# Optimization experiments

Measured on AMD Instinct MI355X. Metric: run time of the kernel, lower is better.

The kernel has to match this reference:

```python
import math
import jax, jax.numpy as jnp
import numpy as np

B, T, L, H = 4, 4096, 4096, 1024


def setup_inputs() -> dict:
    key = jax.random.key(0)
    ks = jax.random.split(key, 12)
    inp = {
        "hidden_states": jax.random.normal(ks[0], (B, T, H), jnp.float32),
        "advisor_states": jax.random.normal(ks[1], (B, L, H), jnp.float32),
        "advisor_ids": jax.random.randint(ks[2], (B, L), 0, 8, jnp.int32),
        "pointer_ids": jax.random.randint(ks[3], (B, T), 0, L - 2, jnp.int32),
    }
    s = 1.0 / math.sqrt(H)
    names = ["Wqj", "Wkj", "Wvj", "Wqi", "Wki", "Wvi", "Wout"]
    for i, n in enumerate(names):
        inp[n] = jax.random.normal(ks[4 + i], (H, H), jnp.float32) * s
    inp["gain"] = jnp.asarray(0.1, jnp.float32)
    inp["council_weights"] = jnp.ones((2,), jnp.float32)
    return inp


def _forward(hidden_states, advisor_states, advisor_ids, pointer_ids,
             Wqj, Wkj, Wvj, Wqi, Wki, Wvi, Wout, gain, council_weights):
    b, t, h = hidden_states.shape
    l = advisor_states.shape[1]
    inv_sqrt_h = 1.0 / math.sqrt(float(h))

    # 3-token advisor window gather: indices [b, t, 3]
    p = pointer_ids[:, :, None]
    indices = jnp.clip(jnp.concatenate([p, p + 1, p + 2], axis=-1), 0, l - 1)
    win_states = jax.vmap(lambda a, idx: a[idx])(advisor_states, indices)  # [b,t,3,h]
    win_ids = jax.vmap(lambda a, idx: a[idx])(advisor_ids, indices)        # [b,t,3]

    # judge head
    qj = hidden_states @ Wqj.T                       # [b,t,h]
    kj = win_states @ Wkj.T                          # [b,t,3,h]
    vj = win_states @ Wvj.T
    sj = jnp.einsum("bth,btwh->btw", qj, kj) * inv_sqrt_h  # [b,t,3]

    # boolean-algebra score surgery on judge scores
    l_rel, l_v1, l_v2 = sj[:, :, 0], sj[:, :, 1], sj[:, :, 2]
    rel_ids = win_ids[:, :, 0]
    is_and = (rel_ids == 0).astype(sj.dtype)
    is_or = (rel_ids == 1).astype(sj.dtype)
    is_not = (rel_ids == 2).astype(sj.dtype)
    is_implies = (rel_ids == 3).astype(sj.dtype)
    is_xor = (rel_ids == 4).astype(sj.dtype)
    l_new = (is_and * (l_v1 + l_v2)
             + is_or * jnp.maximum(l_v1, l_v2)
             + is_not * (-l_v1)
             + is_implies * jnp.maximum(-l_v1, l_v2)
             + is_xor * jnp.abs(l_v1 - l_v2))
    mask_any = jnp.clip(is_and + is_or + is_not + is_implies + is_xor, 0.0, 1.0)
    l_final = mask_any * l_new + (1.0 - mask_any) * l_rel
    sj = jnp.stack([l_final, l_v1, l_v2], axis=-1)

    aj = jax.nn.softmax(sj, axis=-1)
    cj = jnp.einsum("btw,btwh->bth", aj, vj)

    # intuitor head
    qi = hidden_states @ Wqi.T
    ki = win_states @ Wki.T
    vi = win_states @ Wvi.T
    si = jnp.einsum("bth,btwh->btw", qi, ki) * inv_sqrt_h
    ai = jax.nn.softmax(si, axis=-1)
    ci = jnp.einsum("btw,btwh->bth", ai, vi)

    w = jax.nn.softmax(council_weights, axis=0)
    context = w[0] * cj + w[1] * ci
    return (context @ Wout.T) * gain


def reference(hidden_states, advisor_states, advisor_ids, pointer_ids,
              Wqj, Wkj, Wvj, Wqi, Wki, Wvi, Wout, gain, council_weights):
    return _forward(hidden_states, advisor_states, advisor_ids, pointer_ids,
                    Wqj, Wkj, Wvj, Wqi, Wki, Wvi, Wout, gain, council_weights)
```

## Files before the change

kernel.cpp:

```cpp
#include <hip/hip_runtime.h>
#include <hip/hip_bf16.h>
#include <stdint.h>

#define BB 4
#define TT 4096
#define LL 4096
#define HH 1024

typedef __bf16 bf16x8 __attribute__((ext_vector_type(8)));
typedef float f32x4 __attribute__((ext_vector_type(4)));
typedef unsigned short us8v __attribute__((ext_vector_type(8)));
typedef unsigned short us;

__device__ __forceinline__ unsigned short f2b(float f) {
    unsigned u = __builtin_bit_cast(unsigned, f);
    unsigned r = (u + 0x7FFFu + ((u >> 16) & 1u)) >> 16;
    return (unsigned short)r;
}
__device__ __forceinline__ float b2f(unsigned short u) {
    unsigned x = ((unsigned)u) << 16;
    return __builtin_bit_cast(float, x);
}

__device__ __forceinline__ void gload_lds16(const void* g, void* l) {
    __builtin_amdgcn_global_load_lds(
        (const __attribute__((address_space(1))) void*)(uintptr_t)g,
        (__attribute__((address_space(3))) void*)(uintptr_t)l,
        16, 0, 0);
}

__global__ __launch_bounds__(256) void cvt_f32_bf16_k(const float4* __restrict__ src,
                                                      ushort4* __restrict__ dst, int n4) {
    int i = blockIdx.x * 256 + threadIdx.x;
    if (i >= n4) return;
    float4 v = src[i];
    ushort4 o;
    o.x = f2b(v.x); o.y = f2b(v.y); o.z = f2b(v.z); o.w = f2b(v.w);
    dst[i] = o;
}

struct TrArgs { const float* s[6]; unsigned short* d[6]; };
__global__ __launch_bounds__(256) void transp6_cvt_k(TrArgs ta) {
    __shared__ float tile[32][33];
    const int z = blockIdx.z;
    const float* src = ta.s[z];
    unsigned short* dst = ta.d[z];
    const int lx = threadIdx.x & 31, ly = threadIdx.x >> 5;
    const int R = blockIdx.y * 32, C = blockIdx.x * 32;
#pragma unroll
    for (int rr = 0; rr < 4; rr++)
        tile[ly + rr * 8][lx] = src[(size_t)(R + ly + rr * 8) * HH + C + lx];
    __syncthreads();
#pragma unroll
    for (int rr = 0; rr < 4; rr++)
        dst[(size_t)(C + ly + rr * 8) * HH + R + lx] = f2b(tile[lx][ly + rr * 8]);
}

struct FoldArgs { const us* A[4]; const us* B[4]; us* D[4]; };
__global__ __launch_bounds__(256) void gemm_fold4(FoldArgs fa) {
    const int K = 1024;
    __shared__ unsigned short ldsA[128 * 64];
    __shared__ unsigned short ldsB[128 * 64];

    const int z = blockIdx.z;
    const us* A = fa.A[z];
    const us* Bw = fa.B[z];
    us* dst = fa.D[z];

    const int tid = threadIdx.x;
    const int wave = tid >> 6, lane = tid & 63;
    const int m0 = blockIdx.y * 128, n0 = blockIdx.x * 128;
    const int wr = wave >> 1, wc = wave & 1;

    f32x4 acc[4][4];
#pragma unroll
    for (int m = 0; m < 4; m++)
#pragma unroll
        for (int n = 0; n < 4; n++) acc[m][n] = (f32x4)(0.0f);

    const us* Ab = A + (size_t)m0 * K;
    const us* Bb = Bw + (size_t)n0 * K;
    const int rbase = tid >> 3;
    const int col0 = (((tid & 7) ^ (rbase & 7)) << 3);

    for (int k0 = 0; k0 < K; k0 += 64) {
#pragma unroll
        for (int r = 0; r < 4; r++) {
            const int row = r * 32 + rbase;
            gload_lds16(Ab + (size_t)row * K + k0 + col0, &ldsA[r * 2048 + wave * 512]);
            gload_lds16(Bb + (size_t)row * K + k0 + col0, &ldsB[r * 2048 + wave * 512]);
        }
        __syncthreads();

        const int lr = lane & 15, hi = lane >> 4;
        const int sw = (lr & 7) << 4;
        const int c0 = ((hi * 16) ^ sw) >> 1;
        const int c1 = ((64 + hi * 16) ^ sw) >> 1;
        bf16x8 a0[4], a1[4], b0[4], b1[4];
#pragma unroll
        for (int m = 0; m < 4; m++) {
            const int row = (wr * 64 + m * 16 + lr) * 64;
            a0[m] = *reinterpret_cast<const bf16x8*>(&ldsA[row + c0]);
            a1[m] = *reinterpret_cast<const bf16x8*>(&ldsA[row + c1]);
        }
#pragma unroll
        for (int n = 0; n < 4; n++) {
            const int row = (wc * 64 + n * 16 + lr) * 64;
            b0[n] = *reinterpret_cast<const bf16x8*>(&ldsB[row + c0]);
            b1[n] = *reinterpret_cast<const bf16x8*>(&ldsB[row + c1]);
        }
#pragma unroll
        for (int m = 0; m < 4; m++)
#pragma unroll
            for (int n = 0; n < 4; n++)
                acc[m][n] = __builtin_amdgcn_mfma_f32_16x16x32_bf16(a0[m], b0[n], acc[m][n], 0, 0, 0);
#pragma unroll
        for (int m = 0; m < 4; m++)
#pragma unroll
            for (int n = 0; n < 4; n++)
                acc[m][n] = __builtin_amdgcn_mfma_f32_16x16x32_bf16(a1[m], b1[n], acc[m][n], 0, 0, 0);
        __syncthreads();
    }

    const int cc = lane & 15, cr = (lane >> 4) * 4;
#pragma unroll
    for (int m = 0; m < 4; m++)
#pragma unroll
        for (int n = 0; n < 4; n++)
#pragma unroll
            for (int r = 0; r < 4; r++) {
                const int row = m0 + wr * 64 + m * 16 + cr + r;
                const int col = n0 + wc * 64 + n * 16 + cc;
                dst[(size_t)row * 1024 + col] = f2b(acc[m][n][r]);
            }
}

__device__ __forceinline__ void mfma32(const bf16x8 a[8], const bf16x8 b[4], f32x4 acc[8][4]) {
    __builtin_amdgcn_s_setprio(1);
#pragma unroll
    for (int m = 0; m < 8; m++)
#pragma unroll
        for (int n = 0; n < 4; n++)
            acc[m][n] = __builtin_amdgcn_mfma_f32_16x16x32_bf16(a[m], b[n], acc[m][n], 0, 0, 0);
    __builtin_amdgcn_s_setprio(0);
}

#define STAGE2(chunk, src, kcol) \
    { _Pragma("unroll") for (int r_ = 0; r_ < 2; r_++) \
        gload_lds16((src) + (size_t)srow[r_] * K + (kcol) + scol[r_], (chunk) + r_ * 4096 + wave * 512); }

#define RD_A8(cA) \
    { _Pragma("unroll") for (int m_ = 0; m_ < 8; m_++) \
        a[m_] = *reinterpret_cast<const bf16x8*>((cA) + offA + m_ * 512); }

#define RD_B4(cB) \
    { _Pragma("unroll") for (int n_ = 0; n_ < 4; n_++) \
        b[n_] = *reinterpret_cast<const bf16x8*>((cB) + offB + n_ * 512); }

#define BAR __builtin_amdgcn_s_barrier()
#define SB0 __builtin_amdgcn_sched_barrier(0)
#define VMW4 asm volatile("s_waitcnt vmcnt(4)" ::: "memory")
#define VMW0 asm volatile("s_waitcnt vmcnt(0)" ::: "memory")
#define NOWAIT

#define HALF(cA, cB, nA, nB, kn, STG, WAIT)                  \
  {                                                           \
    RD_A8(cA); RD_B4(cB);                                     \
    if (STG) { STAGE2(nA, Ablk, (kn)); STAGE2(nB, Bblk, (kn)); } \
    mfma32(a, b, acc);                                        \
    WAIT;                                                     \
    BAR; SB0;                                                 \
  }

__global__ __launch_bounds__(512, 2) void gemm256(const us* __restrict__ A,
                                                  const us* __restrict__ Bw,
                                                  us* __restrict__ C,
                                                  int M, int N, int K, int gx) {
    __shared__ us lds[65536];

    const int nwg = gridDim.x;
    const int bid = blockIdx.x;
    const int swz = (bid & 7) * (nwg >> 3) + (bid >> 3);
    const int bx = swz % gx, by = swz / gx;
    const int m0 = by * 256, n0 = bx * 256;

    const int tid = threadIdx.x;
    const int wave = tid >> 6, lane = tid & 63;
    const int wr = wave >> 2, wc = wave & 3;
    const int lr = lane & 15, hi = lane >> 4;

    int srow[2], scol[2];
#pragma unroll
    for (int r = 0; r < 2; r++) {
        const int q = r * 64 + (tid >> 3);
        const int s = (tid & 7) ^ (q & 7);
        srow[r] = 2 * q + (s >> 2);
        scol[r] = (s & 3) * 8;
    }
    const us* Ablk = A + (size_t)m0 * K;
    const us* Bblk = Bw + (size_t)n0 * K;

    const int rA = wr * 128 + lr;
    const int offA = (rA >> 1) * 64 + (((((rA & 1) << 2) + hi) ^ ((rA >> 1) & 7)) << 3);
    const int rB = wc * 64 + lr;
    const int offB = (rB >> 1) * 64 + (((((rB & 1) << 2) + hi) ^ ((rB >> 1) & 7)) << 3);

    f32x4 acc[8][4];
#pragma unroll
    for (int m = 0; m < 8; m++)
#pragma unroll
        for (int n = 0; n < 4; n++) acc[m][n] = (f32x4)(0.0f);

    us* cA0 = lds;          us* cA1 = lds + 8192;
    us* cB0 = lds + 16384;  us* cB1 = lds + 24576;
    us* nA0 = lds + 32768;  us* nA1 = lds + 40960;
    us* nB0 = lds + 49152;  us* nB1 = lds + 57344;

    bf16x8 a[8], b[4];

    STAGE2(cA0, Ablk, 0);
    STAGE2(cB0, Bblk, 0);
    STAGE2(cA1, Ablk, 32);
    STAGE2(cB1, Bblk, 32);
    VMW4;
    BAR; SB0;

    const int NT = K >> 6;
    for (int t = 0; t < NT - 1; ++t) {
        const int kn = (t + 1) << 6;
        HALF(cA0, cB0, nA0, nB0, kn, true, VMW4);
        HALF(cA1, cB1, nA1, nB1, kn + 32, true, VMW4);
        us* s0 = cA0; cA0 = nA0; nA0 = s0;
        us* s1 = cA1; cA1 = nA1; nA1 = s1;
        us* s2 = cB0; cB0 = nB0; nB0 = s2;
        us* s3 = cB1; cB1 = nB1; nB1 = s3;
    }
    HALF(cA0, cB0, nA0, nB0, 0, false, VMW0);
    HALF(cA1, cB1, nA1, nB1, 0, false, NOWAIT);

    const int crow0 = m0 + wr * 128 + hi * 4;
    const int ccol0 = n0 + wc * 64 + lr;
#pragma unroll
    for (int mi = 0; mi < 8; mi++)
#pragma unroll
        for (int ni = 0; ni < 4; ni++)
#pragma unroll
            for (int rr = 0; rr < 4; rr++)
                C[(size_t)(crow0 + mi * 16 + rr) * N + ccol0 + ni * 16] = f2b(acc[mi][ni][rr]);
}

__global__ __launch_bounds__(256) void attn_k(const float* __restrict__ HS,
                                              const unsigned short* __restrict__ KV,
                                              const int* __restrict__ adv_ids,
                                              const int* __restrict__ ptr_ids,
                                              const float* __restrict__ council,
                                              const float* __restrict__ gain_p,
                                              float* __restrict__ out) {
    const int wave = threadIdx.x >> 6, lane = threadIdx.x & 63;
    const int gid = blockIdx.x * 4 + wave;
    const int b = gid >> 12, t = gid & 4095;

    const int p = ptr_ids[b * TT + t];
    int idx[3];
#pragma unroll
    for (int w = 0; w < 3; w++) {
        int v = p + w;
        idx[w] = v < (LL - 1) ? v : (LL - 1);
        if (idx[w] < 0) idx[w] = 0;
    }
    const int rel = adv_ids[b * LL + idx[0]];

    float qf[16];
    {
        const f32x4* hrow = reinterpret_cast<const f32x4*>(HS + (size_t)gid * 1024 + lane * 16);
#pragma unroll
        for (int v = 0; v < 4; v++) {
            f32x4 x = hrow[v];
            qf[v * 4 + 0] = x[0]; qf[v * 4 + 1] = x[1]; qf[v * 4 + 2] = x[2]; qf[v * 4 + 3] = x[3];
        }
    }

    float dj[3], di[3];
    us8v vj[3][2], vi[3][2];
#pragma unroll
    for (int w = 0; w < 3; w++) {
        const unsigned short* kvrow = KV + (size_t)(b * LL + idx[w]) * 4096 + lane * 16;
        us8v kj0 = *reinterpret_cast<const us8v*>(kvrow);
        us8v kj1 = *reinterpret_cast<const us8v*>(kvrow + 8);
        vj[w][0] = *reinterpret_cast<const us8v*>(kvrow + 1024);
        vj[w][1] = *reinterpret_cast<const us8v*>(kvrow + 1032);
        us8v ki0 = *reinterpret_cast<const us8v*>(kvrow + 2048);
        us8v ki1 = *reinterpret_cast<const us8v*>(kvrow + 2056);
        vi[w][0] = *reinterpret_cast<const us8v*>(kvrow + 3072);
        vi[w][1] = *reinterpret_cast<const us8v*>(kvrow + 3080);

        float a = 0.f, c = 0.f;
#pragma unroll
        for (int e = 0; e < 8; e++) {
            a += qf[e] * b2f(kj0[e]) + qf[8 + e] * b2f(kj1[e]);
            c += qf[e] * b2f(ki0[e]) + qf[8 + e] * b2f(ki1[e]);
        }
        dj[w] = a;
        di[w] = c;
    }

#pragma unroll
    for (int off = 32; off > 0; off >>= 1) {
#pragma unroll
        for (int w = 0; w < 3; w++) {
            dj[w] += __shfl_xor(dj[w], off, 64);
            di[w] += __shfl_xor(di[w], off, 64);
        }
    }
    float sj[3], si[3];
#pragma unroll
    for (int w = 0; w < 3; w++) {
        sj[w] = dj[w] * 0.03125f;
        si[w] = di[w] * 0.03125f;
    }

    const float l1 = sj[1], l2 = sj[2];
    float lf;
    switch (rel) {
        case 0: lf = l1 + l2; break;
        case 1: lf = fmaxf(l1, l2); break;
        case 2: lf = -l1; break;
        case 3: lf = fmaxf(-l1, l2); break;
        case 4: lf = fabsf(l1 - l2); break;
        default: lf = sj[0]; break;
    }

    float mj = fmaxf(lf, fmaxf(l1, l2));
    float ej0 = expf(lf - mj), ej1 = expf(l1 - mj), ej2 = expf(l2 - mj);
    float invj = 1.0f / (ej0 + ej1 + ej2);
    float aj0 = ej0 * invj, aj1 = ej1 * invj, aj2 = ej2 * invj;

    float mi2 = fmaxf(si[0], fmaxf(si[1], si[2]));
    float ei0 = expf(si[0] - mi2), ei1 = expf(si[1] - mi2), ei2 = expf(si[2] - mi2);
    float invi = 1.0f / (ei0 + ei1 + ei2);
    float ai0 = ei0 * invi, ai1 = ei1 * invi, ai2 = ei2 * invi;

    float c0 = council[0], c1 = council[1];
    float cm = fmaxf(c0, c1);
    float w0 = expf(c0 - cm), w1 = expf(c1 - cm);
    float wsum = 1.0f / (w0 + w1);
    w0 *= wsum; w1 *= wsum;
    const float g = *gain_p;

    float* dst = out + (size_t)gid * 1024 + lane * 16;
#pragma unroll
    for (int h = 0; h < 2; h++) {
        f32x4 o0, o1;
#pragma unroll
        for (int e = 0; e < 8; e++) {
            float cj = aj0 * b2f(vj[0][h][e]) + aj1 * b2f(vj[1][h][e]) + aj2 * b2f(vj[2][h][e]);
            float ci = ai0 * b2f(vi[0][h][e]) + ai1 * b2f(vi[1][h][e]) + ai2 * b2f(vi[2][h][e]);
            float val = (w0 * cj + w1 * ci) * g;
            if (e < 4) o0[e] = val; else o1[e - 4] = val;
        }
        f32x4* dv = reinterpret_cast<f32x4*>(dst + h * 8);
        dv[0] = o0;
        dv[1] = o1;
    }
}

extern "C" void kernel_launch(void* const* d_in, const int* in_sizes, int n_in,
                              void* d_out, int out_size, void* d_ws, size_t ws_size,
                              hipStream_t stream) {
    const float* hs      = (const float*)d_in[0];
    const float* adv     = (const float*)d_in[1];
    const int*   adv_ids = (const int*)d_in[2];
    const int*   ptr_ids = (const int*)d_in[3];
    const float* Wqj = (const float*)d_in[4];
    const float* Wkj = (const float*)d_in[5];
    const float* Wvj = (const float*)d_in[6];
    const float* Wqi = (const float*)d_in[7];
    const float* Wki = (const float*)d_in[8];
    const float* Wvi = (const float*)d_in[9];
    const float* Wout = (const float*)d_in[10];
    const float* gain = (const float*)d_in[11];
    const float* council = (const float*)d_in[12];
    float* out = (float*)d_out;

    const size_t WN  = (size_t)HH * HH;
    const size_t NHb = (size_t)TT * HH;
    dim3 blk(256);

    auto cvt = [&](const float* s, unsigned short* d, size_t n) {
        int n4 = (int)(n / 4);
        cvt_f32_bf16_k<<<dim3(n4 / 256), blk, 0, stream>>>((const float4*)s, (ushort4*)d, n4);
    };

    char* ws = (char*)d_ws;
    unsigned short* Wkv   = (unsigned short*)ws;  ws += WN * 4 * 2;
    unsigned short* WoutB = (unsigned short*)ws;  ws += WN * 2;
    unsigned short* WT    = (unsigned short*)ws;  ws += WN * 6 * 2;

    cvt(Wout, WoutB, WN);
    TrArgs ta;
    ta.s[0] = Wqj; ta.d[0] = WT;
    ta.s[1] = Wkj; ta.d[1] = WT + WN;
    ta.s[2] = Wqi; ta.d[2] = WT + 2 * WN;
    ta.s[3] = Wki; ta.d[3] = WT + 3 * WN;
    ta.s[4] = Wvj; ta.d[4] = WT + 4 * WN;
    ta.s[5] = Wvi; ta.d[5] = WT + 5 * WN;
    transp6_cvt_k<<<dim3(32, 32, 6), blk, 0, stream>>>(ta);

    FoldArgs fa;
    fa.A[0] = WT;          fa.B[0] = WT + WN;     fa.D[0] = Wkv;
    fa.A[1] = WoutB;       fa.B[1] = WT + 4 * WN; fa.D[1] = Wkv + WN;
    fa.A[2] = WT + 2 * WN; fa.B[2] = WT + 3 * WN; fa.D[2] = Wkv + 2 * WN;
    fa.A[3] = WoutB;       fa.B[3] = WT + 5 * WN; fa.D[3] = Wkv + 3 * WN;
    gemm_fold4<<<dim3(8, 8, 4), blk, 0, stream>>>(fa);

    const size_t full_need = (size_t)(24 * 1024 * 1024) + (NHb * BB) * 2
                           + (size_t)16384 * 4096 * 2;

    if (ws_size >= full_need) {
        unsigned short* advb = (unsigned short*)ws;  ws += NHb * BB * 2;
        unsigned short* KVb  = (unsigned short*)ws;

        cvt(adv, advb, NHb * BB);
        gemm256<<<dim3(16 * 64), dim3(512), 0, stream>>>(advb, Wkv, KVb, 16384, 4096, 1024, 16);
        attn_k<<<dim3((BB * TT) / 4), blk, 0, stream>>>(hs, KVb, adv_ids, ptr_ids,
                                                        council, gain, out);
    } else {
        unsigned short* advb = (unsigned short*)ws;  ws += NHb * 2;
        unsigned short* KVb  = (unsigned short*)ws;

        for (int b = 0; b < BB; b++) {
            cvt(adv + (size_t)b * NHb, advb, NHb);
            gemm256<<<dim3(16 * 16), dim3(512), 0, stream>>>(advb, Wkv, KVb, LL, 4096, 1024, 16);
            attn_k<<<dim3(TT / 4), blk, 0, stream>>>(hs + (size_t)b * NHb, KVb,
                                                     adv_ids + b * LL, ptr_ids + b * TT,
                                                     council, gain, out + (size_t)b * NHb);
        }
    }
}
```

Baseline: 268.4 us.

## Bucket-sort tokens by pointer to improve KV gather locality in attention

Adds a small per-batch kernel that counting-sorts token indices into buckets of eight pointer positions. The attention kernel then handles tokens in that order instead of sequence order. Waves running close together therefore gather overlapping KV window rows, which should raise L2 and last-level cache reuse for the random 3-row gathers. It also switches the hidden-state row loads to nontemporal loads so they do not pollute the cache. The cost is an extra launch, an indirection load per wave, and output rows written in scattered order.

```diff
diff --git a/kernel.cpp b/kernel.cpp
--- a/kernel.cpp
+++ b/kernel.cpp
@@ -249,18 +249,55 @@
                 C[(size_t)(crow0 + mi * 16 + rr) * N + ccol0 + ni * 16] = f2b(acc[mi][ni][rr]);
 }
 
+__global__ __launch_bounds__(512) void bucket_perm_k(const int* __restrict__ ptr_ids,
+                                                     int* __restrict__ perm) {
+    __shared__ int hist[512];
+    __shared__ int base[512];
+    const int b = blockIdx.x, tid = threadIdx.x;
+
+    hist[tid] = 0;
+    __syncthreads();
+    for (int i = tid; i < TT; i += 512) {
+        int p = ptr_ids[b * TT + i];
+        p = p < 0 ? 0 : (p > LL - 2 ? LL - 2 : p);
+        atomicAdd(&hist[p >> 3], 1);
+    }
+    __syncthreads();
+    const int cnt = hist[tid];
+    for (int d = 1; d < 512; d <<= 1) {
+        int v = (tid >= d) ? hist[tid - d] : 0;
+        __syncthreads();
+        hist[tid] += v;
+        __syncthreads();
+    }
+    base[tid] = hist[tid] - cnt;
+    __syncthreads();
+    hist[tid] = 0;
+    __syncthreads();
+    for (int i = tid; i < TT; i += 512) {
+        int p = ptr_ids[b * TT + i];
+        p = p < 0 ? 0 : (p > LL - 2 ? LL - 2 : p);
+        const int bkt = p >> 3;
+        const int pos = base[bkt] + atomicAdd(&hist[bkt], 1);
+        perm[b * TT + pos] = i;
+    }
+}
+
 __global__ __launch_bounds__(256) void attn_k(const float* __restrict__ HS,
                                               const unsigned short* __restrict__ KV,
                                               const int* __restrict__ adv_ids,
                                               const int* __restrict__ ptr_ids,
+                                              const int* __restrict__ perm,
                                               const float* __restrict__ council,
                                               const float* __restrict__ gain_p,
                                               float* __restrict__ out) {
     const int wave = threadIdx.x >> 6, lane = threadIdx.x & 63;
-    const int gid = blockIdx.x * 4 + wave;
-    const int b = gid >> 12, t = gid & 4095;
-
-    const int p = ptr_ids[b * TT + t];
+    const int slot = blockIdx.x * 4 + wave;
+    const int b = slot >> 12;
+    const int t = perm[slot];
+    const int gid = b * TT + t;
+
+    const int p = ptr_ids[gid];
     int idx[3];
 #pragma unroll
     for (int w = 0; w < 3; w++) {
@@ -275,7 +312,7 @@
         const f32x4* hrow = reinterpret_cast<const f32x4*>(HS + (size_t)gid * 1024 + lane * 16);
 #pragma unroll
         for (int v = 0; v < 4; v++) {
-            f32x4 x = hrow[v];
+            f32x4 x = __builtin_nontemporal_load(hrow + v);
             qf[v * 4 + 0] = x[0]; qf[v * 4 + 1] = x[1]; qf[v * 4 + 2] = x[2]; qf[v * 4 + 3] = x[3];
         }
     }
@@ -395,6 +432,7 @@
     unsigned short* Wkv   = (unsigned short*)ws;  ws += WN * 4 * 2;
     unsigned short* WoutB = (unsigned short*)ws;  ws += WN * 2;
     unsigned short* WT    = (unsigned short*)ws;  ws += WN * 6 * 2;
+    int* perm             = (int*)ws;             ws += (size_t)BB * TT * 4;
 
     cvt(Wout, WoutB, WN);
     TrArgs ta;
@@ -413,7 +451,9 @@
     fa.A[3] = WoutB;       fa.B[3] = WT + 5 * WN; fa.D[3] = Wkv + 3 * WN;
     gemm_fold4<<<dim3(8, 8, 4), blk, 0, stream>>>(fa);
 
-    const size_t full_need = (size_t)(24 * 1024 * 1024) + (NHb * BB) * 2
+    bucket_perm_k<<<dim3(BB), dim3(512), 0, stream>>>(ptr_ids, perm);
+
+    const size_t full_need = (size_t)(25 * 1024 * 1024) + (NHb * BB) * 2
                            + (size_t)16384 * 4096 * 2;
 
     if (ws_size >= full_need) {
@@ -422,7 +462,7 @@
 
         cvt(adv, advb, NHb * BB);
         gemm256<<<dim3(16 * 64), dim3(512), 0, stream>>>(advb, Wkv, KVb, 16384, 4096, 1024, 16);
-        attn_k<<<dim3((BB * TT) / 4), blk, 0, stream>>>(hs, KVb, adv_ids, ptr_ids,
+        attn_k<<<dim3((BB * TT) / 4), blk, 0, stream>>>(hs, KVb, adv_ids, ptr_ids, perm,
                                                         council, gain, out);
     } else {
         unsigned short* advb = (unsigned short*)ws;  ws += NHb * 2;
@@ -433,6 +473,7 @@
             gemm256<<<dim3(16 * 16), dim3(512), 0, stream>>>(advb, Wkv, KVb, LL, 4096, 1024, 16);
             attn_k<<<dim3(TT / 4), blk, 0, stream>>>(hs + (size_t)b * NHb, KVb,
                                                      adv_ids + b * LL, ptr_ids + b * TT,
+                                                     perm + b * TT,
                                                      council, gain, out + (size_t)b * NHb);
         }
     }
```

Measured after the change: 275.8 us. 2.8% more time.
